# Performance work log

Hardware: AMD Instinct MI355X
Metric: run time of the kernel (lower is better)

The kernel has to match this reference:

```python
import jax, jax.numpy as jnp
import numpy as np

COS_EPS = 1e-08


def setup_inputs() -> dict:
    key = jax.random.key(0)
    k1, k2, k3, k4, k5 = jax.random.split(key, 5)
    B, N, C = 4, 4096, 128
    q_node = jax.random.normal(k1, (B, N, C), dtype=jnp.float32)
    k_node = jax.random.normal(k2, (B, N, C), dtype=jnp.float32)
    v_node = jax.random.normal(k3, (B, N, C), dtype=jnp.float32)
    # shared Linear(h_dim, h_dim): torch default init scale ~ 1/sqrt(C)
    W = jax.random.normal(k4, (C, C), dtype=jnp.float32) / jnp.sqrt(jnp.float32(C))
    b = jax.random.normal(k5, (C,), dtype=jnp.float32) / jnp.sqrt(jnp.float32(C))
    return {"q_node": q_node, "k_node": k_node, "v_node": v_node, "W": W, "b": b}


def reference(q_node, k_node, v_node, W, b):
    # shared projection applied to q, k, v
    q = jnp.einsum('bnc,cd->bnd', q_node, W.T) + b
    k = jnp.einsum('bnc,cd->bnd', k_node, W.T) + b
    v = jnp.einsum('bnc,cd->bnd', v_node, W.T) + b
    # cosine similarity scores: [B, Nq, Nk]
    qn = jnp.linalg.norm(q, axis=2, keepdims=True)        # [B, Nq, 1]
    kn = jnp.linalg.norm(k, axis=2, keepdims=True)        # [B, Nk, 1]
    scores = jnp.einsum('bqc,bkc->bqk', q, k)
    cos_sim = scores / (qn * jnp.swapaxes(kn, 1, 2) + COS_EPS)
    # sum-normalization (not softmax)
    edge_weight = cos_sim / (cos_sim.sum(axis=2, keepdims=True) + 1e-08)
    # weighted aggregation: [B, Nq, C]
    return jnp.einsum('bqk,bkc->bqc', edge_weight, v)
```

## Files before the change

### kernel.cpp

```cpp
#include <hip/hip_runtime.h>

#define BB 4
#define NN 4096
#define CC 128
#define NROWS (BB * NN)

#define QN_OFF  0
#define QP_OFF  (QN_OFF + NROWS)
#define MM_OFF  (QP_OFF + NROWS * CC)
#define KS_OFF  (MM_OFF + BB * CC * CC)
#define PP_OFF  (KS_OFF + BB * CC)
#define KP_OFF  (PP_OFF + 512 * CC * CC)

__device__ __forceinline__ void fma4(float4& a, const float4 x,
    const float4 w0, const float4 w1, const float4 w2, const float4 w3)
{
    a.x += x.x * w0.x + x.y * w1.x + x.z * w2.x + x.w * w3.x;
    a.y += x.x * w0.y + x.y * w1.y + x.z * w2.y + x.w * w3.y;
    a.z += x.x * w0.z + x.y * w1.z + x.z * w2.z + x.w * w3.z;
    a.w += x.x * w0.w + x.y * w1.w + x.z * w2.w + x.w * w3.w;
}

__global__ __launch_bounds__(512, 4) void projpb_kernel(
    const float* __restrict__ q_node, const float* __restrict__ k_node,
    const float* __restrict__ v_node, const float* __restrict__ W,
    const float* __restrict__ bias, float* __restrict__ ws)
{
    __shared__ float S[CC * CC];
    __shared__ float4 red[512];
    const int tid = threadIdx.x;

    for (int e = tid; e < CC * CC; e += 512) {
        int d = e >> 7, c = e & 127;
        S[(c << 7) + ((((d >> 2) ^ (c & 31)) << 2) | (d & 3))] = W[e];
    }

    const int blk  = blockIdx.x;
    const int base = blk * 32;
    const int dg = tid & 31;
    const int rg = tid >> 5;

    float4 bias4 = ((const float4*)bias)[dg];
    float4 acc[4];
#pragma unroll
    for (int i = 0; i < 4; i++) acc[i] = bias4;

    __syncthreads();

    const float4* Qv = (const float4*)(q_node + (size_t)(base + rg * 2) * CC);
    const float4* Kv = (const float4*)(k_node + (size_t)(base + rg * 2) * CC);
    const float4* Sv = (const float4*)S;

#define LW(s0, s1, s2, s3, c)                              \
    s0 = Sv[(((c) + 0) << 5) + (dg ^ (((c) + 0) & 31))];   \
    s1 = Sv[(((c) + 1) << 5) + (dg ^ (((c) + 1) & 31))];   \
    s2 = Sv[(((c) + 2) << 5) + (dg ^ (((c) + 2) & 31))];   \
    s3 = Sv[(((c) + 3) << 5) + (dg ^ (((c) + 3) & 31))];
#define LX(q0, q1, k0, k1, c)                              \
    { const int c4_ = (c) >> 2;                            \
      q0 = Qv[c4_]; q1 = Qv[32 + c4_];                     \
      k0 = Kv[c4_]; k1 = Kv[32 + c4_]; }
#define FM(w0, w1, w2, w3, q0, q1, k0, k1)                 \
    fma4(acc[0], q0, w0, w1, w2, w3);                      \
    fma4(acc[1], q1, w0, w1, w2, w3);                      \
    fma4(acc[2], k0, w0, w1, w2, w3);                      \
    fma4(acc[3], k1, w0, w1, w2, w3);

    float4 wA0, wA1, wA2, wA3, wB0, wB1, wB2, wB3;
    float4 qA0, qA1, kA0, kA1, qB0, qB1, kB0, kB1;

    LW(wA0, wA1, wA2, wA3, 0)
    LX(qA0, qA1, kA0, kA1, 0)
    for (int c = 0; c <= CC - 16; c += 8) {
        LW(wB0, wB1, wB2, wB3, c + 4)
        LX(qB0, qB1, kB0, kB1, c + 4)
        FM(wA0, wA1, wA2, wA3, qA0, qA1, kA0, kA1)
        LW(wA0, wA1, wA2, wA3, c + 8)
        LX(qA0, qA1, kA0, kA1, c + 8)
        FM(wB0, wB1, wB2, wB3, qB0, qB1, kB0, kB1)
    }
    LW(wB0, wB1, wB2, wB3, CC - 4)
    LX(qB0, qB1, kB0, kB1, CC - 4)
    FM(wA0, wA1, wA2, wA3, qA0, qA1, kA0, kA1)
    FM(wB0, wB1, wB2, wB3, qB0, qB1, kB0, kB1)

#undef LW
#undef LX
#undef FM

#pragma unroll
    for (int i = 0; i < 2; i++) {
        const int rq = base + rg * 2 + i;
        float ss = acc[i].x * acc[i].x + acc[i].y * acc[i].y
                 + acc[i].z * acc[i].z + acc[i].w * acc[i].w;
#pragma unroll
        for (int off = 16; off > 0; off >>= 1) ss += __shfl_xor(ss, off, 32);
        ((float4*)(ws + QP_OFF + (size_t)rq * CC))[dg] = acc[i];
        if (dg == 0) ws[QN_OFF + rq] = sqrtf(ss);
    }

    __syncthreads();

    float* Khs = S;
    float* Vs  = S + 4096;

#pragma unroll
    for (int i = 0; i < 2; i++) {
        float ss = acc[2 + i].x * acc[2 + i].x + acc[2 + i].y * acc[2 + i].y
                 + acc[2 + i].z * acc[2 + i].z + acc[2 + i].w * acc[2 + i].w;
#pragma unroll
        for (int off = 16; off > 0; off >>= 1) ss += __shfl_xor(ss, off, 32);
        float inv = 1.0f / sqrtf(ss);
        float4 o = acc[2 + i];
        o.x *= inv; o.y *= inv; o.z *= inv; o.w *= inv;
        ((float4*)(Khs + (rg * 2 + i) * CC))[dg] = o;
    }

    const int c4v = tid & 31, nrv = tid >> 5;
    const float* Vp = v_node + (size_t)base * CC;
#pragma unroll
    for (int i = 0; i < 2; i++) {
        int n = nrv + i * 16;
        ((float4*)(Vs + n * CC))[c4v] = ((const float4*)(Vp + (size_t)n * CC))[c4v];
    }
    __syncthreads();

    float4 ksum4 = make_float4(0.f, 0.f, 0.f, 0.f);
#pragma unroll
    for (int i = 0; i < 2; i++) {
        int n = nrv + i * 16;
        float4 kv = ((const float4*)(Khs + n * CC))[c4v];
        ksum4.x += kv.x; ksum4.y += kv.y; ksum4.z += kv.z; ksum4.w += kv.w;
    }

    const int dg2 = tid & 15, cg = tid >> 4;
    float a2[4][8];
#pragma unroll
    for (int i = 0; i < 4; i++)
#pragma unroll
        for (int j = 0; j < 8; j++) a2[i][j] = 0.f;

#define P2L(ka, va, vb, n)                                  \
    ka = *(const float4*)(Khs + (n) * CC + 4 * cg);         \
    va = *(const float4*)(Vs + (n) * CC + 4 * dg2);         \
    vb = *(const float4*)(Vs + (n) * CC + 64 + 4 * dg2);
#define P2F(ka, va, vb)                                     \
    {  float kc[4] = {ka.x, ka.y, ka.z, ka.w};              \
       float vd[8] = {va.x, va.y, va.z, va.w,               \
                      vb.x, vb.y, vb.z, vb.w};              \
       _Pragma("unroll")                                    \
       for (int i = 0; i < 4; i++)                          \
           { _Pragma("unroll")                              \
             for (int j = 0; j < 8; j++)                    \
                 a2[i][j] += kc[i] * vd[j]; } }

    {
        float4 kaA, vaA, vbA, kaB, vaB, vbB;
        P2L(kaA, vaA, vbA, 0)
        for (int n = 0; n <= 28; n += 2) {
            P2L(kaB, vaB, vbB, n + 1)
            P2F(kaA, vaA, vbA)
            P2L(kaA, vaA, vbA, n + 2)
            P2F(kaB, vaB, vbB)
        }
        P2L(kaB, vaB, vbB, 31)
        P2F(kaA, vaA, vbA)
        P2F(kaB, vaB, vbB)
    }
#undef P2L
#undef P2F

    float* pp = ws + PP_OFF + (size_t)blk * (CC * CC);
#pragma unroll
    for (int i = 0; i < 4; i++) {
        int c = 4 * cg + i;
        *(float4*)(pp + c * CC + 4 * dg2) =
            make_float4(a2[i][0], a2[i][1], a2[i][2], a2[i][3]);
        *(float4*)(pp + c * CC + 64 + 4 * dg2) =
            make_float4(a2[i][4], a2[i][5], a2[i][6], a2[i][7]);
    }

    red[nrv * 32 + c4v] = ksum4;
    __syncthreads();
    if (tid < 32) {
        float4 sm = red[tid];
#pragma unroll
        for (int i = 1; i < 16; i++) {
            float4 t = red[i * 32 + tid];
            sm.x += t.x; sm.y += t.y; sm.z += t.z; sm.w += t.w;
        }
        ((float4*)(ws + KP_OFF + (size_t)blk * CC))[tid] = sm;
    }
}

__global__ __launch_bounds__(256) void mchain_kernel(const float* __restrict__ W,
                                                     const float* __restrict__ bias,
                                                     float* __restrict__ ws)
{
    __shared__ float4 W4s[CC * 32];
    __shared__ float m0row[2][CC];
    __shared__ float kpart[4];
    __shared__ float ksl[2];
    const int tid = threadIdx.x;
    const int b = blockIdx.y, x = blockIdx.x;
    const int c0 = x * 2;

    for (int idx = tid; idx < CC * 32; idx += 256) {
        int e = idx >> 5, d4 = idx & 31;
        W4s[(e << 5) + (d4 ^ (e & 31))] = ((const float4*)W)[idx];
    }

    {
        const int r = tid >> 7, d = tid & 127;
        const float* pp = ws + PP_OFF + (size_t)(b * 128) * (CC * CC)
                        + (size_t)(c0 + r) * CC + d;
        float a0 = 0.f, a1 = 0.f, a2 = 0.f, a3 = 0.f;
#pragma unroll 8
        for (int p = 0; p < 128; p += 4) {
            a0 += pp[(size_t)(p + 0) * (CC * CC)];
            a1 += pp[(size_t)(p + 1) * (CC * CC)];
            a2 += pp[(size_t)(p + 2) * (CC * CC)];
            a3 += pp[(size_t)(p + 3) * (CC * CC)];
        }
        m0row[r][d] = (a0 + a1) + (a2 + a3);
    }

    {
        const int rr = tid >> 7, p = tid & 127;
        float v = ws[KP_OFF + (size_t)(b * 128 + p) * CC + c0 + rr];
#pragma unroll
        for (int off = 32; off > 0; off >>= 1) v += __shfl_xor(v, off, 64);
        if ((tid & 63) == 0) kpart[tid >> 6] = v;
    }
    __syncthreads();
    if (tid < 2) {
        float s = kpart[tid * 2] + kpart[tid * 2 + 1];
        ksl[tid] = s;
        ws[KS_OFF + b * CC + c0 + tid] = s;
    }
    __syncthreads();

    const int r = tid >> 7, e = tid & 127;
    const float4* mr = (const float4*)m0row[r];
    float m = 0.f;
#pragma unroll
    for (int d4 = 0; d4 < 32; d4++) {
        float4 a4 = mr[d4];
        float4 w4 = W4s[(e << 5) + (d4 ^ (e & 31))];
        m += a4.x * w4.x + a4.y * w4.y + a4.z * w4.z + a4.w * w4.w;
    }
    m += ksl[r] * bias[e];
    ws[MM_OFF + (size_t)b * CC * CC + (size_t)(c0 + r) * CC + e] = m;
}

__global__ __launch_bounds__(512, 4) void out_kernel(const float* __restrict__ ws,
                                                     float* __restrict__ out)
{
    __shared__ float Ml[CC * CC];

    const int blk = blockIdx.x;
    const int b = blk >> 7;
    const int r0 = (blk & 127) * 32;
    const float* M = ws + MM_OFF + (size_t)b * CC * CC;
    const int tid = threadIdx.x;

    for (int e = tid; e < CC * CC / 4; e += 512)
        ((float4*)Ml)[e] = ((const float4*)M)[e];

    const float4* Ks4 = (const float4*)(ws + KS_OFF + b * CC);
    const int dg = tid & 31, rg = tid >> 5;
    const int row = r0 + rg * 2;
    const float4* Qv = (const float4*)(ws + QP_OFF + ((size_t)b * NN + row) * CC);
    const float4* Mv = (const float4*)Ml;

    float4 acc[2];
    float s[2];
#pragma unroll
    for (int i = 0; i < 2; i++) {
        acc[i] = make_float4(0.f, 0.f, 0.f, 0.f);
        s[i] = 0.f;
    }

    __syncthreads();

#define OLW(m0, m1, m2, m3, ks, c)               \
    m0 = Mv[(((c) + 0) << 5) + dg];              \
    m1 = Mv[(((c) + 1) << 5) + dg];              \
    m2 = Mv[(((c) + 2) << 5) + dg];              \
    m3 = Mv[(((c) + 3) << 5) + dg];              \
    ks = Ks4[(c) >> 2];
#define OLX(x0, x1, c)                           \
    { const int c4_ = (c) >> 2;                  \
      x0 = Qv[c4_]; x1 = Qv[32 + c4_]; }
#define OFM(m0, m1, m2, m3, ks, x0, x1)                              \
    fma4(acc[0], x0, m0, m1, m2, m3);                                \
    s[0] += x0.x * ks.x + x0.y * ks.y + x0.z * ks.z + x0.w * ks.w;   \
    fma4(acc[1], x1, m0, m1, m2, m3);                                \
    s[1] += x1.x * ks.x + x1.y * ks.y + x1.z * ks.z + x1.w * ks.w;

    {
        float4 mA0, mA1, mA2, mA3, mB0, mB1, mB2, mB3;
        float4 ksA, ksB, xA0, xA1, xB0, xB1;
        OLW(mA0, mA1, mA2, mA3, ksA, 0)
        OLX(xA0, xA1, 0)
        for (int c = 0; c <= CC - 16; c += 8) {
            OLW(mB0, mB1, mB2, mB3, ksB, c + 4)
            OLX(xB0, xB1, c + 4)
            OFM(mA0, mA1, mA2, mA3, ksA, xA0, xA1)
            OLW(mA0, mA1, mA2, mA3, ksA, c + 8)
            OLX(xA0, xA1, c + 8)
            OFM(mB0, mB1, mB2, mB3, ksB, xB0, xB1)
        }
        OLW(mB0, mB1, mB2, mB3, ksB, CC - 4)
        OLX(xB0, xB1, CC - 4)
        OFM(mA0, mA1, mA2, mA3, ksA, xA0, xA1)
        OFM(mB0, mB1, mB2, mB3, ksB, xB0, xB1)
    }
#undef OLW
#undef OLX
#undef OFM

    float* op = out + ((size_t)b * NN + row) * CC;
    const float* qn = ws + QN_OFF + (size_t)b * NN + row;
#pragma unroll
    for (int i = 0; i < 2; i++) {
        float inv = 1.0f / (s[i] + 1e-8f * qn[i]);
        float4 o = acc[i];
        o.x *= inv; o.y *= inv; o.z *= inv; o.w *= inv;
        ((float4*)(op + (size_t)i * CC))[dg] = o;
    }
}

extern "C" void kernel_launch(void* const* d_in, const int* in_sizes, int n_in,
                              void* d_out, int out_size, void* d_ws, size_t ws_size,
                              hipStream_t stream)
{
    const float* q_node = (const float*)d_in[0];
    const float* k_node = (const float*)d_in[1];
    const float* v_node = (const float*)d_in[2];
    const float* W      = (const float*)d_in[3];
    const float* bias   = (const float*)d_in[4];
    float* out = (float*)d_out;
    float* ws  = (float*)d_ws;

    projpb_kernel<<<512, 512, 0, stream>>>(q_node, k_node, v_node, W, bias, ws);
    mchain_kernel<<<dim3(64, BB), 256, 0, stream>>>(W, bias, ws);
    out_kernel<<<512, 512, 0, stream>>>(ws, out);
}
```

Before: 133.6 us.

## Double rows per block in projection and output kernels, halving partial count

Each projection and output block now handles 64 rows instead of 32, with each thread computing 4 rows. Shared-memory W and M tiles are loaded half as often, and the number of per-block K^T V partial matrices that mchain must reduce drops from 128 to 64 per batch. The cost is higher register pressure, lower launch-bounds occupancy, and only 256 blocks on a GPU with many CUs, which may leave some compute units idle.

```diff
diff --git a/kernel.cpp b/kernel.cpp
--- a/kernel.cpp
+++ b/kernel.cpp
@@ -10,7 +10,7 @@
 #define MM_OFF  (QP_OFF + NROWS * CC)
 #define KS_OFF  (MM_OFF + BB * CC * CC)
 #define PP_OFF  (KS_OFF + BB * CC)
-#define KP_OFF  (PP_OFF + 512 * CC * CC)
+#define KP_OFF  (PP_OFF + 256 * CC * CC)
 
 __device__ __forceinline__ void fma4(float4& a, const float4 x,
     const float4 w0, const float4 w1, const float4 w2, const float4 w3)
@@ -21,7 +21,12 @@
     a.w += x.x * w0.w + x.y * w1.w + x.z * w2.w + x.w * w3.w;
 }
 
-__global__ __launch_bounds__(512, 4) void projpb_kernel(
+__device__ __forceinline__ float dot4(const float4 x, const float4 k)
+{
+    return x.x * k.x + x.y * k.y + x.z * k.z + x.w * k.w;
+}
+
+__global__ __launch_bounds__(512, 2) void projpb_kernel(
     const float* __restrict__ q_node, const float* __restrict__ k_node,
     const float* __restrict__ v_node, const float* __restrict__ W,
     const float* __restrict__ bias, float* __restrict__ ws)
@@ -36,19 +41,19 @@
     }
 
     const int blk  = blockIdx.x;
-    const int base = blk * 32;
+    const int base = blk * 64;
     const int dg = tid & 31;
     const int rg = tid >> 5;
 
     float4 bias4 = ((const float4*)bias)[dg];
-    float4 acc[4];
-#pragma unroll
-    for (int i = 0; i < 4; i++) acc[i] = bias4;
-
-    __syncthreads();
-
-    const float4* Qv = (const float4*)(q_node + (size_t)(base + rg * 2) * CC);
-    const float4* Kv = (const float4*)(k_node + (size_t)(base + rg * 2) * CC);
+    float4 acc[8];
+#pragma unroll
+    for (int i = 0; i < 8; i++) acc[i] = bias4;
+
+    __syncthreads();
+
+    const float4* Qv = (const float4*)(q_node + (size_t)(base + rg * 4) * CC);
+    const float4* Kv = (const float4*)(k_node + (size_t)(base + rg * 4) * CC);
     const float4* Sv = (const float4*)S;
 
 #define LW(s0, s1, s2, s3, c)                              \
@@ -56,41 +61,48 @@
     s1 = Sv[(((c) + 1) << 5) + (dg ^ (((c) + 1) & 31))];   \
     s2 = Sv[(((c) + 2) << 5) + (dg ^ (((c) + 2) & 31))];   \
     s3 = Sv[(((c) + 3) << 5) + (dg ^ (((c) + 3) & 31))];
-#define LX(q0, q1, k0, k1, c)                              \
+#define LX(xq, xk, c)                                      \
     { const int c4_ = (c) >> 2;                            \
-      q0 = Qv[c4_]; q1 = Qv[32 + c4_];                     \
-      k0 = Kv[c4_]; k1 = Kv[32 + c4_]; }
-#define FM(w0, w1, w2, w3, q0, q1, k0, k1)                 \
-    fma4(acc[0], q0, w0, w1, w2, w3);                      \
-    fma4(acc[1], q1, w0, w1, w2, w3);                      \
-    fma4(acc[2], k0, w0, w1, w2, w3);                      \
-    fma4(acc[3], k1, w0, w1, w2, w3);
-
-    float4 wA0, wA1, wA2, wA3, wB0, wB1, wB2, wB3;
-    float4 qA0, qA1, kA0, kA1, qB0, qB1, kB0, kB1;
-
-    LW(wA0, wA1, wA2, wA3, 0)
-    LX(qA0, qA1, kA0, kA1, 0)
-    for (int c = 0; c <= CC - 16; c += 8) {
-        LW(wB0, wB1, wB2, wB3, c + 4)
-        LX(qB0, qB1, kB0, kB1, c + 4)
-        FM(wA0, wA1, wA2, wA3, qA0, qA1, kA0, kA1)
-        LW(wA0, wA1, wA2, wA3, c + 8)
-        LX(qA0, qA1, kA0, kA1, c + 8)
-        FM(wB0, wB1, wB2, wB3, qB0, qB1, kB0, kB1)
-    }
-    LW(wB0, wB1, wB2, wB3, CC - 4)
-    LX(qB0, qB1, kB0, kB1, CC - 4)
-    FM(wA0, wA1, wA2, wA3, qA0, qA1, kA0, kA1)
-    FM(wB0, wB1, wB2, wB3, qB0, qB1, kB0, kB1)
-
+      xq[0] = Qv[c4_];      xq[1] = Qv[32 + c4_];          \
+      xq[2] = Qv[64 + c4_]; xq[3] = Qv[96 + c4_];          \
+      xk[0] = Kv[c4_];      xk[1] = Kv[32 + c4_];          \
+      xk[2] = Kv[64 + c4_]; xk[3] = Kv[96 + c4_]; }
+#define FM(w0, w1, w2, w3, xq, xk)                         \
+    fma4(acc[0], xq[0], w0, w1, w2, w3);                   \
+    fma4(acc[1], xq[1], w0, w1, w2, w3);                   \
+    fma4(acc[2], xq[2], w0, w1, w2, w3);                   \
+    fma4(acc[3], xq[3], w0, w1, w2, w3);                   \
+    fma4(acc[4], xk[0], w0, w1, w2, w3);                   \
+    fma4(acc[5], xk[1], w0, w1, w2, w3);                   \
+    fma4(acc[6], xk[2], w0, w1, w2, w3);                   \
+    fma4(acc[7], xk[3], w0, w1, w2, w3);
+
+    {
+        float4 wA0, wA1, wA2, wA3, wB0, wB1, wB2, wB3;
+        float4 xqA[4], xkA[4], xqB[4], xkB[4];
+
+        LW(wA0, wA1, wA2, wA3, 0)
+        LX(xqA, xkA, 0)
+        for (int c = 0; c <= CC - 16; c += 8) {
+            LW(wB0, wB1, wB2, wB3, c + 4)
+            LX(xqB, xkB, c + 4)
+            FM(wA0, wA1, wA2, wA3, xqA, xkA)
+            LW(wA0, wA1, wA2, wA3, c + 8)
+            LX(xqA, xkA, c + 8)
+            FM(wB0, wB1, wB2, wB3, xqB, xkB)
+        }
+        LW(wB0, wB1, wB2, wB3, CC - 4)
+        LX(xqB, xkB, CC - 4)
+        FM(wA0, wA1, wA2, wA3, xqA, xkA)
+        FM(wB0, wB1, wB2, wB3, xqB, xkB)
+    }
 #undef LW
 #undef LX
 #undef FM
 
 #pragma unroll
-    for (int i = 0; i < 2; i++) {
-        const int rq = base + rg * 2 + i;
+    for (int i = 0; i < 4; i++) {
+        const int rq = base + rg * 4 + i;
         float ss = acc[i].x * acc[i].x + acc[i].y * acc[i].y
                  + acc[i].z * acc[i].z + acc[i].w * acc[i].w;
 #pragma unroll
@@ -102,24 +114,24 @@
     __syncthreads();
 
     float* Khs = S;
-    float* Vs  = S + 4096;
-
-#pragma unroll
-    for (int i = 0; i < 2; i++) {
-        float ss = acc[2 + i].x * acc[2 + i].x + acc[2 + i].y * acc[2 + i].y
-                 + acc[2 + i].z * acc[2 + i].z + acc[2 + i].w * acc[2 + i].w;
+    float* Vs  = S + 8192;
+
+#pragma unroll
+    for (int i = 0; i < 4; i++) {
+        float ss = acc[4 + i].x * acc[4 + i].x + acc[4 + i].y * acc[4 + i].y
+                 + acc[4 + i].z * acc[4 + i].z + acc[4 + i].w * acc[4 + i].w;
 #pragma unroll
         for (int off = 16; off > 0; off >>= 1) ss += __shfl_xor(ss, off, 32);
         float inv = 1.0f / sqrtf(ss);
-        float4 o = acc[2 + i];
+        float4 o = acc[4 + i];
         o.x *= inv; o.y *= inv; o.z *= inv; o.w *= inv;
-        ((float4*)(Khs + (rg * 2 + i) * CC))[dg] = o;
+        ((float4*)(Khs + (rg * 4 + i) * CC))[dg] = o;
     }
 
     const int c4v = tid & 31, nrv = tid >> 5;
     const float* Vp = v_node + (size_t)base * CC;
 #pragma unroll
-    for (int i = 0; i < 2; i++) {
+    for (int i = 0; i < 4; i++) {
         int n = nrv + i * 16;
         ((float4*)(Vs + n * CC))[c4v] = ((const float4*)(Vp + (size_t)n * CC))[c4v];
     }
@@ -127,7 +139,7 @@
 
     float4 ksum4 = make_float4(0.f, 0.f, 0.f, 0.f);
 #pragma unroll
-    for (int i = 0; i < 2; i++) {
+    for (int i = 0; i < 4; i++) {
         int n = nrv + i * 16;
         float4 kv = ((const float4*)(Khs + n * CC))[c4v];
         ksum4.x += kv.x; ksum4.y += kv.y; ksum4.z += kv.z; ksum4.w += kv.w;
@@ -157,13 +169,13 @@
     {
         float4 kaA, vaA, vbA, kaB, vaB, vbB;
         P2L(kaA, vaA, vbA, 0)
-        for (int n = 0; n <= 28; n += 2) {
+        for (int n = 0; n <= 60; n += 2) {
             P2L(kaB, vaB, vbB, n + 1)
             P2F(kaA, vaA, vbA)
             P2L(kaA, vaA, vbA, n + 2)
             P2F(kaB, vaB, vbB)
         }
-        P2L(kaB, vaB, vbB, 31)
+        P2L(kaB, vaB, vbB, 63)
         P2F(kaA, vaA, vbA)
         P2F(kaB, vaB, vbB)
     }
@@ -212,11 +224,11 @@
 
     {
         const int r = tid >> 7, d = tid & 127;
-        const float* pp = ws + PP_OFF + (size_t)(b * 128) * (CC * CC)
+        const float* pp = ws + PP_OFF + (size_t)(b * 64) * (CC * CC)
                         + (size_t)(c0 + r) * CC + d;
         float a0 = 0.f, a1 = 0.f, a2 = 0.f, a3 = 0.f;
 #pragma unroll 8
-        for (int p = 0; p < 128; p += 4) {
+        for (int p = 0; p < 64; p += 4) {
             a0 += pp[(size_t)(p + 0) * (CC * CC)];
             a1 += pp[(size_t)(p + 1) * (CC * CC)];
             a2 += pp[(size_t)(p + 2) * (CC * CC)];
@@ -227,7 +239,8 @@
 
     {
         const int rr = tid >> 7, p = tid & 127;
-        float v = ws[KP_OFF + (size_t)(b * 128 + p) * CC + c0 + rr];
+        float v = 0.f;
+        if (p < 64) v = ws[KP_OFF + (size_t)(b * 64 + p) * CC + c0 + rr];
 #pragma unroll
         for (int off = 32; off > 0; off >>= 1) v += __shfl_xor(v, off, 64);
         if ((tid & 63) == 0) kpart[tid >> 6] = v;
@@ -253,14 +266,14 @@
     ws[MM_OFF + (size_t)b * CC * CC + (size_t)(c0 + r) * CC + e] = m;
 }
 
-__global__ __launch_bounds__(512, 4) void out_kernel(const float* __restrict__ ws,
+__global__ __launch_bounds__(512, 2) void out_kernel(const float* __restrict__ ws,
                                                      float* __restrict__ out)
 {
     __shared__ float Ml[CC * CC];
 
     const int blk = blockIdx.x;
-    const int b = blk >> 7;
-    const int r0 = (blk & 127) * 32;
+    const int b = blk >> 6;
+    const int r0 = (blk & 63) * 64;
     const float* M = ws + MM_OFF + (size_t)b * CC * CC;
     const int tid = threadIdx.x;
 
@@ -269,14 +282,14 @@
 
     const float4* Ks4 = (const float4*)(ws + KS_OFF + b * CC);
     const int dg = tid & 31, rg = tid >> 5;
-    const int row = r0 + rg * 2;
+    const int row = r0 + rg * 4;
     const float4* Qv = (const float4*)(ws + QP_OFF + ((size_t)b * NN + row) * CC);
     const float4* Mv = (const float4*)Ml;
 
-    float4 acc[2];
-    float s[2];
-#pragma unroll
-    for (int i = 0; i < 2; i++) {
+    float4 acc[4];
+    float s[4];
+#pragma unroll
+    for (int i = 0; i < 4; i++) {
         acc[i] = make_float4(0.f, 0.f, 0.f, 0.f);
         s[i] = 0.f;
     }
@@ -289,32 +302,34 @@
     m2 = Mv[(((c) + 2) << 5) + dg];              \
     m3 = Mv[(((c) + 3) << 5) + dg];              \
     ks = Ks4[(c) >> 2];
-#define OLX(x0, x1, c)                           \
-    { const int c4_ = (c) >> 2;                  \
-      x0 = Qv[c4_]; x1 = Qv[32 + c4_]; }
-#define OFM(m0, m1, m2, m3, ks, x0, x1)                              \
-    fma4(acc[0], x0, m0, m1, m2, m3);                                \
-    s[0] += x0.x * ks.x + x0.y * ks.y + x0.z * ks.z + x0.w * ks.w;   \
-    fma4(acc[1], x1, m0, m1, m2, m3);                                \
-    s[1] += x1.x * ks.x + x1.y * ks.y + x1.z * ks.z + x1.w * ks.w;
+#define OLX(xv, c)                                 \
+    { const int c4_ = (c) >> 2;                    \
+      xv[0] = Qv[c4_];      xv[1] = Qv[32 + c4_];  \
+      xv[2] = Qv[64 + c4_]; xv[3] = Qv[96 + c4_]; }
+#define OFM(m0, m1, m2, m3, ks, xv)                  \
+    _Pragma("unroll")                                \
+    for (int i_ = 0; i_ < 4; i_++) {                 \
+        fma4(acc[i_], xv[i_], m0, m1, m2, m3);       \
+        s[i_] += dot4(xv[i_], ks);                   \
+    }
 
     {
         float4 mA0, mA1, mA2, mA3, mB0, mB1, mB2, mB3;
-        float4 ksA, ksB, xA0, xA1, xB0, xB1;
+        float4 ksA, ksB, xA[4], xB[4];
         OLW(mA0, mA1, mA2, mA3, ksA, 0)
-        OLX(xA0, xA1, 0)
+        OLX(xA, 0)
         for (int c = 0; c <= CC - 16; c += 8) {
             OLW(mB0, mB1, mB2, mB3, ksB, c + 4)
-            OLX(xB0, xB1, c + 4)
-            OFM(mA0, mA1, mA2, mA3, ksA, xA0, xA1)
+            OLX(xB, c + 4)
+            OFM(mA0, mA1, mA2, mA3, ksA, xA)
             OLW(mA0, mA1, mA2, mA3, ksA, c + 8)
-            OLX(xA0, xA1, c + 8)
-            OFM(mB0, mB1, mB2, mB3, ksB, xB0, xB1)
+            OLX(xA, c + 8)
+            OFM(mB0, mB1, mB2, mB3, ksB, xB)
         }
         OLW(mB0, mB1, mB2, mB3, ksB, CC - 4)
-        OLX(xB0, xB1, CC - 4)
-        OFM(mA0, mA1, mA2, mA3, ksA, xA0, xA1)
-        OFM(mB0, mB1, mB2, mB3, ksB, xB0, xB1)
+        OLX(xB, CC - 4)
+        OFM(mA0, mA1, mA2, mA3, ksA, xA)
+        OFM(mB0, mB1, mB2, mB3, ksB, xB)
     }
 #undef OLW
 #undef OLX
@@ -323,7 +338,7 @@
     float* op = out + ((size_t)b * NN + row) * CC;
     const float* qn = ws + QN_OFF + (size_t)b * NN + row;
 #pragma unroll
-    for (int i = 0; i < 2; i++) {
+    for (int i = 0; i < 4; i++) {
         float inv = 1.0f / (s[i] + 1e-8f * qn[i]);
         float4 o = acc[i];
         o.x *= inv; o.y *= inv; o.z *= inv; o.w *= inv;
@@ -343,7 +358,7 @@
     float* out = (float*)d_out;
     float* ws  = (float*)d_ws;
 
-    projpb_kernel<<<512, 512, 0, stream>>>(q_node, k_node, v_node, W, bias, ws);
+    projpb_kernel<<<256, 512, 0, stream>>>(q_node, k_node, v_node, W, bias, ws);
     mchain_kernel<<<dim3(64, BB), 256, 0, stream>>>(W, bias, ws);
-    out_kernel<<<512, 512, 0, stream>>>(ws, out);
-}
+    out_kernel<<<256, 512, 0, stream>>>(ws, out);
+}
```

Result: faster. 130.6 us (-2.3%).
